# Kernel tuning notes

Hardware: AMD Instinct MI355X
Metric: run time of the kernel (lower is better)

Reference implementation:

```python
import jax, jax.numpy as jnp
import numpy as np

EMB = 768
HEADS = 12
HD = EMB // HEADS
DFF = 4 * EMB
EPS = 1e-5


def layernorm(x, g, b):
    mu = jnp.mean(x, axis=-1, keepdims=True)
    var = jnp.mean(jnp.square(x - mu), axis=-1, keepdims=True)
    return (x - mu) * jax.lax.rsqrt(var + EPS) * g + b


def setup_inputs() -> dict:
    key = jax.random.key(0)
    ks = jax.random.split(key, 12)
    B, L = 16, 1024
    std = 0.02
    return {
        "x": jax.random.normal(ks[0], (B, L, EMB), jnp.float32),
        "ln1_g": jnp.ones((EMB,), jnp.float32),
        "ln1_b": jnp.zeros((EMB,), jnp.float32),
        "Wq": jax.random.normal(ks[1], (EMB, EMB), jnp.float32) * std,
        "bq": jnp.zeros((EMB,), jnp.float32),
        "Wk": jax.random.normal(ks[2], (EMB, EMB), jnp.float32) * std,
        "bk": jnp.zeros((EMB,), jnp.float32),
        "Wv": jax.random.normal(ks[3], (EMB, EMB), jnp.float32) * std,
        "bv": jnp.zeros((EMB,), jnp.float32),
        "Wo": jax.random.normal(ks[4], (EMB, EMB), jnp.float32) * std,
        "bo": jnp.zeros((EMB,), jnp.float32),
        "ln2_g": jnp.ones((EMB,), jnp.float32),
        "ln2_b": jnp.zeros((EMB,), jnp.float32),
        "W1": jax.random.normal(ks[5], (EMB, DFF), jnp.float32) * std,
        "b1": jnp.zeros((DFF,), jnp.float32),
        "W2": jax.random.normal(ks[6], (DFF, EMB), jnp.float32) * std,
        "b2": jnp.zeros((EMB,), jnp.float32),
    }


def reference(x, ln1_g, ln1_b, Wq, bq, Wk, bk, Wv, bv, Wo, bo,
              ln2_g, ln2_b, W1, b1, W2, b2):
    B, L, D = x.shape
    # --- attention (pre-LN) ---
    h = layernorm(x, ln1_g, ln1_b)
    q = (h @ Wq + bq).reshape(B, L, HEADS, HD)
    k = (h @ Wk + bk).reshape(B, L, HEADS, HD)
    v = (h @ Wv + bv).reshape(B, L, HEADS, HD)
    scores = jnp.einsum("blhd,bmhd->bhlm", q, k) / np.sqrt(HD).astype(np.float32)
    attn = jax.nn.softmax(scores, axis=-1)
    ctx = jnp.einsum("bhlm,bmhd->blhd", attn, v).reshape(B, L, D)
    x = x + ctx @ Wo + bo
    # --- MLP (pre-LN), dropout is identity in eval ---
    h = layernorm(x, ln2_g, ln2_b)
    h = jax.nn.gelu(h @ W1 + b1, approximate=False)  # torch nn.GELU default = exact erf
    x = x + h @ W2 + b2
    return x
```

## Files before the change

### kernel.cpp

```cpp
#include <hip/hip_runtime.h>
#include <hip/hip_bf16.h>
#include <math.h>

#define EMB 768
#define DFF 3072
#define HEADS 12
#define HD 64
#define LSEQ 1024
#define BATCH 16
#define BL (BATCH * LSEQ)
#define QKVD 2304
#define QSCALE 0.1803368801111204f

typedef __attribute__((ext_vector_type(8))) short short8;
typedef __attribute__((ext_vector_type(4))) float floatx4;
typedef unsigned short u16;

__device__ __forceinline__ u16 f2bf(float f) {
  union { float f; unsigned u; } c; c.f = f;
  unsigned u = c.u;
  u += 0x7fffu + ((u >> 16) & 1u);
  return (u16)(u >> 16);
}
__device__ __forceinline__ u16 f2bf_trunc(float f) {
  union { float f; unsigned u; } c; c.f = f;
  return (u16)(c.u >> 16);
}
__device__ __forceinline__ float fast_exp2(float x) {
#if __has_builtin(__builtin_amdgcn_exp2f)
  return __builtin_amdgcn_exp2f(x);
#else
  return exp2f(x);
#endif
}
__device__ __forceinline__ float fast_rcp(float x) {
#if __has_builtin(__builtin_amdgcn_rcpf)
  return __builtin_amdgcn_rcpf(x);
#else
  return 1.0f / x;
#endif
}
__device__ __forceinline__ float gelu_fast(float x) {
  float x2 = x * x;
  float u = x * fmaf(0.10294540f, x2, 2.30211423f);
  u = fminf(fmaxf(u, -30.f), 30.f);
  float t = fast_exp2(u);
  return x * t * fast_rcp(t + 1.0f);
}
__device__ __forceinline__ void async16(const u16* g, u16* l) {
  __builtin_amdgcn_global_load_lds(
      (const __attribute__((address_space(1))) unsigned int*)g,
      (__attribute__((address_space(3))) unsigned int*)l, 16, 0, 0);
}

__global__ __launch_bounds__(256) void ln_kernel(const float* __restrict__ x,
                                                 const float* __restrict__ g,
                                                 const float* __restrict__ b,
                                                 u16* __restrict__ out) {
  int row = blockIdx.x * 4 + (threadIdx.x >> 6);
  int lane = threadIdx.x & 63;
  const float* xr = x + (size_t)row * EMB;
  float v[12];
#pragma unroll
  for (int i = 0; i < 3; i++) {
    float4 t = *reinterpret_cast<const float4*>(xr + i * 256 + lane * 4);
    v[i*4+0] = t.x; v[i*4+1] = t.y; v[i*4+2] = t.z; v[i*4+3] = t.w;
  }
  float s = 0.f, ss = 0.f;
#pragma unroll
  for (int i = 0; i < 12; i++) { s += v[i]; ss += v[i] * v[i]; }
#pragma unroll
  for (int off = 1; off < 64; off <<= 1) {
    s  += __shfl_xor(s, off);
    ss += __shfl_xor(ss, off);
  }
  float mu  = s * (1.f / 768.f);
  float var = ss * (1.f / 768.f) - mu * mu;
  float rs  = rsqrtf(var + 1e-5f);
  u16* orow = out + (size_t)row * EMB;
#pragma unroll
  for (int i = 0; i < 3; i++) {
    int col = i * 256 + lane * 4;
    ushort4 o;
    o.x = f2bf((v[i*4+0] - mu) * rs * g[col+0] + b[col+0]);
    o.y = f2bf((v[i*4+1] - mu) * rs * g[col+1] + b[col+1]);
    o.z = f2bf((v[i*4+2] - mu) * rs * g[col+2] + b[col+2]);
    o.w = f2bf((v[i*4+3] - mu) * rs * g[col+3] + b[col+3]);
    *reinterpret_cast<ushort4*>(orow + col) = o;
  }
}

__global__ void wt_kernel(const float* __restrict__ in, u16* __restrict__ out,
                          int K, int N) {
  __shared__ float t[32][33];
  int x0 = blockIdx.x * 32;
  int y0 = blockIdx.y * 32;
  int tx = threadIdx.x, ty = threadIdx.y;
#pragma unroll
  for (int i = 0; i < 4; i++)
    t[ty + i*8][tx] = in[(size_t)(y0 + ty + i*8) * N + x0 + tx];
  __syncthreads();
#pragma unroll
  for (int i = 0; i < 4; i++)
    out[(size_t)(x0 + ty + i*8) * K + y0 + tx] = f2bf(t[tx][ty + i*8]);
}

__global__ void bias_cat(const float* __restrict__ bq, const float* __restrict__ bk,
                         const float* __restrict__ bv, float* __restrict__ o) {
  int i = blockIdx.x * 256 + threadIdx.x;
  if (i >= QKVD) return;
  o[i] = i < EMB ? bq[i] : (i < 2*EMB ? bk[i - EMB] : bv[i - 2*EMB]);
}

__global__ void vtrans_kernel(const u16* __restrict__ qkv, u16* __restrict__ vt) {
  __shared__ u16 t[32][33];
  int l0 = blockIdx.x * 32;
  int d0 = blockIdx.y * 32;
  int bh = blockIdx.z;
  int b = bh / HEADS, h = bh % HEADS;
  int tx = threadIdx.x, ty = threadIdx.y;
#pragma unroll
  for (int i = 0; i < 4; i++)
    t[ty + i*8][tx] = qkv[(size_t)(b * LSEQ + l0 + ty + i*8) * QKVD + 2*EMB + h * HD + d0 + tx];
  __syncthreads();
#pragma unroll
  for (int i = 0; i < 4; i++)
    vt[(size_t)(bh * HD + d0 + ty + i*8) * LSEQ + l0 + tx] = t[tx][ty + i*8];
}

#define BK 64
__global__ __launch_bounds__(256) void gemm_kernel(
    const u16* __restrict__ A, const u16* __restrict__ Bt,
    const float* __restrict__ bias, const float* __restrict__ res,
    u16* __restrict__ outb, float* __restrict__ outf,
    int M, int N, int K, int mode, float scale, int scale_n) {
  __shared__ u16 As[128 * BK];
  __shared__ u16 Bs[128 * BK];
  int tid = threadIdx.x;
  int lane = tid & 63, wave = tid >> 6;
  int wm = wave & 1, wn = wave >> 1;
  int l16 = lane & 15, lhi = lane >> 4;
  int m0 = blockIdx.x * 128, n0 = blockIdx.y * 128;

  floatx4 acc[4][4];
#pragma unroll
  for (int i = 0; i < 4; i++)
#pragma unroll
    for (int j = 0; j < 4; j++) acc[i][j] = {0.f, 0.f, 0.f, 0.f};

  int rr = lane >> 3;
  int cs = ((lane & 7) ^ rr) * 8;
  const u16* aptr = A + (size_t)(m0 + wave * 32 + rr) * K + cs;
  const u16* bptr = Bt + (size_t)(n0 + wave * 32 + rr) * K + cs;
  u16* asl = As + (wave * 32) * BK;
  u16* bsl = Bs + (wave * 32) * BK;

  int l7 = l16 & 7;
  int oa0 = (wm * 64 + l16) * BK + ((lhi ^ l7) * 8);
  int ob0 = (wn * 64 + l16) * BK + ((lhi ^ l7) * 8);
  int oa1 = oa0 ^ 32;
  int ob1 = ob0 ^ 32;

  for (int k0 = 0; k0 < K; k0 += BK) {
    __syncthreads();
#pragma unroll
    for (int i = 0; i < 4; i++) {
      async16(aptr + (size_t)(i * 8) * K + k0, asl + i * 8 * BK);
      async16(bptr + (size_t)(i * 8) * K + k0, bsl + i * 8 * BK);
    }
    __syncthreads();
#pragma unroll
    for (int kk = 0; kk < 2; kk++) {
      int oA = kk ? oa1 : oa0;
      int oB = kk ? ob1 : ob0;
      short8 af[4], bfr[4];
#pragma unroll
      for (int mt = 0; mt < 4; mt++)
        af[mt] = *reinterpret_cast<const short8*>(&As[oA + mt * 16 * BK]);
#pragma unroll
      for (int nt = 0; nt < 4; nt++)
        bfr[nt] = *reinterpret_cast<const short8*>(&Bs[oB + nt * 16 * BK]);
#pragma unroll
      for (int mt = 0; mt < 4; mt++)
#pragma unroll
        for (int nt = 0; nt < 4; nt++)
          acc[mt][nt] = __builtin_amdgcn_mfma_f32_16x16x32_bf16(af[mt], bfr[nt],
                                                                acc[mt][nt], 0, 0, 0);
    }
  }

#pragma unroll
  for (int mt = 0; mt < 4; mt++) {
#pragma unroll
    for (int nt = 0; nt < 4; nt++) {
      int n = n0 + wn*64 + nt*16 + l16;
      float bv = bias[n];
      float sc = (n < scale_n) ? scale : 1.0f;
#pragma unroll
      for (int r = 0; r < 4; r++) {
        int m = m0 + wm*64 + mt*16 + lhi*4 + r;
        float val = acc[mt][nt][r] + bv;
        if (mode == 2) val = gelu_fast(val);
        if (mode == 1) {
          outf[(size_t)m * N + n] = val + res[(size_t)m * N + n];
        } else {
          outb[(size_t)m * N + n] = f2bf(val * sc);
        }
      }
    }
  }
}

__global__ __launch_bounds__(256) void flash_kernel(
    const u16* __restrict__ qkv, const u16* __restrict__ vt,
    u16* __restrict__ ctx) {
  __shared__ u16 Qs[64][72], Ks[64][72], Vs[64][72];
  __shared__ u16 Ps[4][16][72];
  int tid = threadIdx.x;
  int lane = tid & 63, w = tid >> 6;
  int l16 = lane & 15, lhi = lane >> 4;
  int l0 = blockIdx.x * 64;
  int h = blockIdx.y, b = blockIdx.z;

  const u16* q = qkv + h * HD;
  const u16* k = qkv + EMB + h * HD;

  int srow = tid >> 3;
  int scol = (tid & 7) * 8;
#pragma unroll
  for (int i = 0; i < 2; i++) {
    int row = srow + i * 32;
    *reinterpret_cast<int4*>(&Qs[row][scol]) =
        *reinterpret_cast<const int4*>(q + (size_t)(b*LSEQ + l0 + row)*QKVD + scol);
  }

  float l_i[4] = {0.f, 0.f, 0.f, 0.f};
  floatx4 o[4];
#pragma unroll
  for (int nt = 0; nt < 4; nt++) o[nt] = {0.f, 0.f, 0.f, 0.f};

  for (int kt = 0; kt < LSEQ; kt += 64) {
    __syncthreads();
#pragma unroll
    for (int i = 0; i < 2; i++) {
      int row = srow + i * 32;
      *reinterpret_cast<int4*>(&Ks[row][scol]) =
          *reinterpret_cast<const int4*>(k + (size_t)(b*LSEQ + kt + row)*QKVD + scol);
      *reinterpret_cast<int4*>(&Vs[row][scol]) =
          *reinterpret_cast<const int4*>(vt + (size_t)((b*HEADS + h)*HD + row)*LSEQ + kt + scol);
    }
    __syncthreads();

    floatx4 s[4];
#pragma unroll
    for (int nt = 0; nt < 4; nt++) s[nt] = {0.f, 0.f, 0.f, 0.f};
    short8 aq[2];
#pragma unroll
    for (int kk = 0; kk < 2; kk++)
      aq[kk] = *reinterpret_cast<const short8*>(&Qs[w*16 + l16][kk*32 + lhi*8]);
#pragma unroll
    for (int nt = 0; nt < 4; nt++)
#pragma unroll
      for (int kk = 0; kk < 2; kk++) {
        short8 bk = *reinterpret_cast<const short8*>(&Ks[nt*16 + l16][kk*32 + lhi*8]);
        s[nt] = __builtin_amdgcn_mfma_f32_16x16x32_bf16(aq[kk], bk, s[nt], 0, 0, 0);
      }

#pragma unroll
    for (int nt = 0; nt < 4; nt++)
#pragma unroll
      for (int r = 0; r < 4; r++)
        s[nt][r] = fast_exp2(s[nt][r]);
#pragma unroll
    for (int r = 0; r < 4; r++)
      l_i[r] += (s[0][r] + s[1][r]) + (s[2][r] + s[3][r]);

#pragma unroll
    for (int nt = 0; nt < 4; nt++)
#pragma unroll
      for (int r = 0; r < 4; r++)
        Ps[w][lhi*4 + r][nt*16 + l16] = f2bf_trunc(s[nt][r]);
    short8 ap[2];
#pragma unroll
    for (int kk = 0; kk < 2; kk++)
      ap[kk] = *reinterpret_cast<const short8*>(&Ps[w][l16][kk*32 + lhi*8]);
#pragma unroll
    for (int nt = 0; nt < 4; nt++)
#pragma unroll
      for (int kk = 0; kk < 2; kk++) {
        short8 bv = *reinterpret_cast<const short8*>(&Vs[nt*16 + l16][kk*32 + lhi*8]);
        o[nt] = __builtin_amdgcn_mfma_f32_16x16x32_bf16(ap[kk], bv, o[nt], 0, 0, 0);
      }
  }

#pragma unroll
  for (int off = 1; off < 16; off <<= 1)
#pragma unroll
    for (int r = 0; r < 4; r++)
      l_i[r] += __shfl_xor(l_i[r], off);

#pragma unroll
  for (int r = 0; r < 4; r++) {
    float inv = fast_rcp(l_i[r]);
    int grow = b*LSEQ + l0 + w*16 + lhi*4 + r;
#pragma unroll
    for (int nt = 0; nt < 4; nt++)
      ctx[(size_t)grow * EMB + h*HD + nt*16 + l16] = f2bf(o[nt][r] * inv);
  }
}

extern "C" void kernel_launch(void* const* d_in, const int* in_sizes, int n_in,
                              void* d_out, int out_size, void* d_ws, size_t ws_size,
                              hipStream_t stream) {
  const float* x    = (const float*)d_in[0];
  const float* ln1g = (const float*)d_in[1];
  const float* ln1b = (const float*)d_in[2];
  const float* Wq   = (const float*)d_in[3];
  const float* bq   = (const float*)d_in[4];
  const float* Wk   = (const float*)d_in[5];
  const float* bk   = (const float*)d_in[6];
  const float* Wv   = (const float*)d_in[7];
  const float* bv   = (const float*)d_in[8];
  const float* Wo   = (const float*)d_in[9];
  const float* bo   = (const float*)d_in[10];
  const float* ln2g = (const float*)d_in[11];
  const float* ln2b = (const float*)d_in[12];
  const float* W1   = (const float*)d_in[13];
  const float* b1   = (const float*)d_in[14];
  const float* W2   = (const float*)d_in[15];
  const float* b2   = (const float*)d_in[16];

  char* ws = (char*)d_ws;
  u16* qkv_bf = (u16*)(ws);
  u16* vt_bf  = (u16*)(ws + (size_t)75497472);
  u16* h_bf   = (u16*)(ws + (size_t)100663296);
  float* x2   = (float*)(ws + (size_t)125829120);
  u16* m_bf   = (u16*)(ws);
  char* wp = ws + (size_t)176160768;
  u16* wqkv = (u16*)(wp);
  u16* wot  = (u16*)(wp + (size_t)3538944);
  u16* w1t  = (u16*)(wp + (size_t)3538944 + 1179648);
  u16* w2t  = (u16*)(wp + (size_t)3538944 + 1179648 + 4718592);
  float* qkvbias = (float*)(wp + (size_t)3538944 + 1179648 + 2*4718592);

  dim3 b256(256), tb(32, 8);

  wt_kernel<<<dim3(24, 24), tb, 0, stream>>>(Wq, wqkv,               EMB, EMB);
  wt_kernel<<<dim3(24, 24), tb, 0, stream>>>(Wk, wqkv + 768*768,     EMB, EMB);
  wt_kernel<<<dim3(24, 24), tb, 0, stream>>>(Wv, wqkv + 2*768*768,   EMB, EMB);
  wt_kernel<<<dim3(24, 24), tb, 0, stream>>>(Wo, wot, EMB, EMB);
  wt_kernel<<<dim3(96, 24), tb, 0, stream>>>(W1, w1t, EMB, DFF);
  wt_kernel<<<dim3(24, 96), tb, 0, stream>>>(W2, w2t, DFF, EMB);
  bias_cat<<<dim3(9), b256, 0, stream>>>(bq, bk, bv, qkvbias);

  ln_kernel<<<dim3(BL/4), b256, 0, stream>>>(x, ln1g, ln1b, h_bf);

  gemm_kernel<<<dim3(128, 18), b256, 0, stream>>>(h_bf, wqkv, qkvbias, nullptr,
      qkv_bf, nullptr, BL, QKVD, EMB, 0, QSCALE, EMB);

  vtrans_kernel<<<dim3(32, 2, BATCH*HEADS), tb, 0, stream>>>(qkv_bf, vt_bf);

  flash_kernel<<<dim3(LSEQ/64, HEADS, BATCH), b256, 0, stream>>>(qkv_bf, vt_bf, h_bf);

  gemm_kernel<<<dim3(128, 6), b256, 0, stream>>>(h_bf, wot, bo, x, nullptr, x2,
      BL, EMB, EMB, 1, 1.0f, 0);

  ln_kernel<<<dim3(BL/4), b256, 0, stream>>>(x2, ln2g, ln2b, h_bf);

  gemm_kernel<<<dim3(128, 24), b256, 0, stream>>>(h_bf, w1t, b1, nullptr, m_bf,
      nullptr, BL, DFF, EMB, 2, 1.0f, 0);

  gemm_kernel<<<dim3(128, 6), b256, 0, stream>>>(m_bf, w2t, b2, x2, nullptr,
      (float*)d_out, BL, EMB, DFF, 1, 1.0f, 0);
}
```

Before: 645.9 us.

## Restructure flash attention to load K/V fragments directly into registers per wave

The flash kernel no longer stages Q, K and V in shared memory with block-wide barriers. Each wave now owns 64 query rows kept in registers and loads K and V MFMA fragments straight from global memory. It computes S^T = K·Q^T so P can be written with vector stores into a double-buffered per-wave LDS tile. The grid is flattened to 768 blocks with a swizzled mapping so blocks sharing a batch-head run close together for L2 reuse. This removes the __syncthreads and LDS traffic for K and V, but each wave now fetches K and V separately, which raises global and L2 load volume and register pressure.

After: 624.3 us. 3.3% less time.

```diff
diff --git a/kernel.cpp b/kernel.cpp
--- a/kernel.cpp
+++ b/kernel.cpp
@@ -51,6 +51,9 @@
   __builtin_amdgcn_global_load_lds(
       (const __attribute__((address_space(1))) unsigned int*)g,
       (__attribute__((address_space(3))) unsigned int*)l, 16, 0, 0);
+}
+__device__ __forceinline__ short8 load16(const u16* p) {
+  return *reinterpret_cast<const short8*>(p);
 }
 
 __global__ __launch_bounds__(256) void ln_kernel(const float* __restrict__ x,
@@ -211,101 +214,102 @@
   }
 }
 
+#define PSTRIDE 76
 __global__ __launch_bounds__(256) void flash_kernel(
     const u16* __restrict__ qkv, const u16* __restrict__ vt,
     u16* __restrict__ ctx) {
-  __shared__ u16 Qs[64][72], Ks[64][72], Vs[64][72];
-  __shared__ u16 Ps[4][16][72];
+  __shared__ u16 Ps[4][2][16][PSTRIDE];
   int tid = threadIdx.x;
   int lane = tid & 63, w = tid >> 6;
   int l16 = lane & 15, lhi = lane >> 4;
-  int l0 = blockIdx.x * 64;
-  int h = blockIdx.y, b = blockIdx.z;
-
-  const u16* q = qkv + h * HD;
-  const u16* k = qkv + EMB + h * HD;
-
-  int srow = tid >> 3;
-  int scol = (tid & 7) * 8;
-#pragma unroll
-  for (int i = 0; i < 2; i++) {
-    int row = srow + i * 32;
-    *reinterpret_cast<int4*>(&Qs[row][scol]) =
-        *reinterpret_cast<const int4*>(q + (size_t)(b*LSEQ + l0 + row)*QKVD + scol);
-  }
-
+
+  int i = blockIdx.x;
+  int bh = (i & 7) | ((i >> 5) << 3);
+  int qb = (i >> 3) & 3;
+  int b = bh / HEADS, h = bh % HEADS;
+  int q0 = qb * 256 + w * 64;
+
+  const u16* qbase = qkv + (size_t)(b * LSEQ) * QKVD + h * HD;
+  const u16* kbase = qbase + EMB;
+  const u16* vbase = vt + (size_t)(bh * HD) * LSEQ;
+
+  short8 qf[4][2];
+#pragma unroll
+  for (int st = 0; st < 4; st++)
+#pragma unroll
+    for (int kk = 0; kk < 2; kk++)
+      qf[st][kk] = load16(qbase + (size_t)(q0 + st*16 + l16) * QKVD + kk*32 + lhi*8);
+
+  floatx4 o[4][4];
+#pragma unroll
+  for (int st = 0; st < 4; st++)
+#pragma unroll
+    for (int mt = 0; mt < 4; mt++) o[st][mt] = {0.f, 0.f, 0.f, 0.f};
   float l_i[4] = {0.f, 0.f, 0.f, 0.f};
-  floatx4 o[4];
-#pragma unroll
-  for (int nt = 0; nt < 4; nt++) o[nt] = {0.f, 0.f, 0.f, 0.f};
 
   for (int kt = 0; kt < LSEQ; kt += 64) {
-    __syncthreads();
-#pragma unroll
-    for (int i = 0; i < 2; i++) {
-      int row = srow + i * 32;
-      *reinterpret_cast<int4*>(&Ks[row][scol]) =
-          *reinterpret_cast<const int4*>(k + (size_t)(b*LSEQ + kt + row)*QKVD + scol);
-      *reinterpret_cast<int4*>(&Vs[row][scol]) =
-          *reinterpret_cast<const int4*>(vt + (size_t)((b*HEADS + h)*HD + row)*LSEQ + kt + scol);
-    }
-    __syncthreads();
-
-    floatx4 s[4];
-#pragma unroll
-    for (int nt = 0; nt < 4; nt++) s[nt] = {0.f, 0.f, 0.f, 0.f};
-    short8 aq[2];
-#pragma unroll
-    for (int kk = 0; kk < 2; kk++)
-      aq[kk] = *reinterpret_cast<const short8*>(&Qs[w*16 + l16][kk*32 + lhi*8]);
-#pragma unroll
-    for (int nt = 0; nt < 4; nt++)
+    short8 kf[4][2], vf[4][2];
+#pragma unroll
+    for (int mt = 0; mt < 4; mt++)
 #pragma unroll
       for (int kk = 0; kk < 2; kk++) {
-        short8 bk = *reinterpret_cast<const short8*>(&Ks[nt*16 + l16][kk*32 + lhi*8]);
-        s[nt] = __builtin_amdgcn_mfma_f32_16x16x32_bf16(aq[kk], bk, s[nt], 0, 0, 0);
+        kf[mt][kk] = load16(kbase + (size_t)(kt + mt*16 + l16) * QKVD + kk*32 + lhi*8);
+        vf[mt][kk] = load16(vbase + (size_t)(mt*16 + l16) * LSEQ + kt + kk*32 + lhi*8);
       }
 
 #pragma unroll
-    for (int nt = 0; nt < 4; nt++)
-#pragma unroll
-      for (int r = 0; r < 4; r++)
-        s[nt][r] = fast_exp2(s[nt][r]);
-#pragma unroll
-    for (int r = 0; r < 4; r++)
-      l_i[r] += (s[0][r] + s[1][r]) + (s[2][r] + s[3][r]);
-
-#pragma unroll
-    for (int nt = 0; nt < 4; nt++)
-#pragma unroll
-      for (int r = 0; r < 4; r++)
-        Ps[w][lhi*4 + r][nt*16 + l16] = f2bf_trunc(s[nt][r]);
-    short8 ap[2];
-#pragma unroll
-    for (int kk = 0; kk < 2; kk++)
-      ap[kk] = *reinterpret_cast<const short8*>(&Ps[w][l16][kk*32 + lhi*8]);
-#pragma unroll
-    for (int nt = 0; nt < 4; nt++)
-#pragma unroll
-      for (int kk = 0; kk < 2; kk++) {
-        short8 bv = *reinterpret_cast<const short8*>(&Vs[nt*16 + l16][kk*32 + lhi*8]);
-        o[nt] = __builtin_amdgcn_mfma_f32_16x16x32_bf16(ap[kk], bv, o[nt], 0, 0, 0);
+    for (int st = 0; st < 4; st++) {
+      u16* pbuf = &Ps[w][st & 1][0][0];
+      floatx4 s[4];
+#pragma unroll
+      for (int mt = 0; mt < 4; mt++) s[mt] = {0.f, 0.f, 0.f, 0.f};
+#pragma unroll
+      for (int mt = 0; mt < 4; mt++)
+#pragma unroll
+        for (int kk = 0; kk < 2; kk++)
+          s[mt] = __builtin_amdgcn_mfma_f32_16x16x32_bf16(kf[mt][kk], qf[st][kk],
+                                                          s[mt], 0, 0, 0);
+      float ls = 0.f;
+#pragma unroll
+      for (int mt = 0; mt < 4; mt++) {
+        ushort4 pw;
+        float p0 = fast_exp2(s[mt][0]), p1 = fast_exp2(s[mt][1]);
+        float p2 = fast_exp2(s[mt][2]), p3 = fast_exp2(s[mt][3]);
+        ls += (p0 + p1) + (p2 + p3);
+        pw.x = f2bf_trunc(p0); pw.y = f2bf_trunc(p1);
+        pw.z = f2bf_trunc(p2); pw.w = f2bf_trunc(p3);
+        *reinterpret_cast<ushort4*>(&pbuf[l16 * PSTRIDE + mt*16 + lhi*4]) = pw;
       }
-  }
-
-#pragma unroll
-  for (int off = 1; off < 16; off <<= 1)
-#pragma unroll
-    for (int r = 0; r < 4; r++)
-      l_i[r] += __shfl_xor(l_i[r], off);
-
-#pragma unroll
-  for (int r = 0; r < 4; r++) {
-    float inv = fast_rcp(l_i[r]);
-    int grow = b*LSEQ + l0 + w*16 + lhi*4 + r;
-#pragma unroll
-    for (int nt = 0; nt < 4; nt++)
-      ctx[(size_t)grow * EMB + h*HD + nt*16 + l16] = f2bf(o[nt][r] * inv);
+      l_i[st] += ls;
+      short8 pf0 = load16(&pbuf[l16 * PSTRIDE + 0*32 + lhi*8]);
+      short8 pf1 = load16(&pbuf[l16 * PSTRIDE + 1*32 + lhi*8]);
+#pragma unroll
+      for (int mt = 0; mt < 4; mt++) {
+        o[st][mt] = __builtin_amdgcn_mfma_f32_16x16x32_bf16(vf[mt][0], pf0,
+                                                            o[st][mt], 0, 0, 0);
+        o[st][mt] = __builtin_amdgcn_mfma_f32_16x16x32_bf16(vf[mt][1], pf1,
+                                                            o[st][mt], 0, 0, 0);
+      }
+    }
+  }
+
+#pragma unroll
+  for (int st = 0; st < 4; st++) {
+    l_i[st] += __shfl_xor(l_i[st], 16);
+    l_i[st] += __shfl_xor(l_i[st], 32);
+  }
+
+#pragma unroll
+  for (int st = 0; st < 4; st++) {
+    float inv = fast_rcp(l_i[st]);
+    size_t rowbase = (size_t)(b * LSEQ + q0 + st*16 + l16) * EMB + h * HD;
+#pragma unroll
+    for (int mt = 0; mt < 4; mt++) {
+      ushort4 ow;
+      ow.x = f2bf(o[st][mt][0] * inv); ow.y = f2bf(o[st][mt][1] * inv);
+      ow.z = f2bf(o[st][mt][2] * inv); ow.w = f2bf(o[st][mt][3] * inv);
+      *reinterpret_cast<ushort4*>(&ctx[rowbase + mt*16 + lhi*4]) = ow;
+    }
   }
 }
 
@@ -360,7 +364,7 @@
 
   vtrans_kernel<<<dim3(32, 2, BATCH*HEADS), tb, 0, stream>>>(qkv_bf, vt_bf);
 
-  flash_kernel<<<dim3(LSEQ/64, HEADS, BATCH), b256, 0, stream>>>(qkv_bf, vt_bf, h_bf);
+  flash_kernel<<<dim3(768), b256, 0, stream>>>(qkv_bf, vt_bf, h_bf);
 
   gemm_kernel<<<dim3(128, 6), b256, 0, stream>>>(h_bf, wot, bo, x, nullptr, x2,
       BL, EMB, EMB, 1, 1.0f, 0);
```
